# Optimization experiments

Measured on AMD Instinct MI355X. Metric: run time of the kernel, lower is better.

Reference implementation:

```python
import jax, jax.numpy as jnp
import numpy as np

B, N1, N2, E = 8, 32, 32, 256
H = 8                 # num_heads == args.vir_heads
KD = E // H           # key dim per head = 32
HD = E // H           # head dim (value_dim == embed_dim)
L = N1 * N2           # 1024 tokens
SCALING = KD ** -0.5
LN_EPS = 1e-5


def _rel_pos_2d():
    # RetNetRelPosDeform2D with zero offsets (vir_use_deformable=False)
    half = 1.0 / 10000.0 ** jnp.linspace(0.0, 1.0, KD // 2)
    angle = jnp.repeat(half, 2)                                   # (KD,) interleaved pairs
    decay = jnp.log(1.0 - 2.0 ** (-2.0 - 5.0 * jnp.arange(H, dtype=jnp.float32) / H))  # (H,)
    i1 = jnp.arange(N1, dtype=jnp.float32)
    i2 = jnp.arange(N2, dtype=jnp.float32)
    index_k = (i1[:, None] + i2[None, :]).reshape(L)              # (L,)
    sin_k = jnp.sin(index_k[:, None] * angle[None, :])            # (L, KD)
    cos_k = jnp.cos(index_k[:, None] * angle[None, :])
    # zero offsets => index_q == index_k, broadcast over (B, H)
    sin_q = sin_k[None, None]                                     # (1,1,L,KD)
    cos_q = cos_k[None, None]
    # Manhattan distance decay mask on the 2D grid
    d = (jnp.abs(i1[:, None, None, None] - i1[None, None, :, None])
         + jnp.abs(i2[None, :, None, None] - i2[None, None, None, :])).reshape(L, L)
    mask = jnp.exp(d[None, :, :] * decay[:, None, None])          # (H, L, L)
    mask = jnp.nan_to_num(mask)
    mask = mask / jnp.sqrt(mask.sum(-1, keepdims=True))
    return sin_q, cos_q, sin_k, cos_k, mask


def rotate_every_two(x):
    x1 = x[..., ::2]
    x2 = x[..., 1::2]
    return jnp.stack((-x2, x1), axis=-1).reshape(x.shape)


def theta_shift(x, sin, cos):
    return x * cos + rotate_every_two(x) * sin


def setup_inputs() -> dict:
    key = jax.random.key(0)
    ks = jax.random.split(key, 5)
    gain_qkv = 2.0 ** -2.5 * (6.0 / (E + E)) ** 0.5  # xavier_uniform bound scale
    gain_o = 2.0 ** -1 * (6.0 / (E + E)) ** 0.5
    x = jax.random.normal(ks[0], (B, N1, N2, E), dtype=jnp.float32)
    Wq = jax.random.uniform(ks[1], (E, E), jnp.float32, -gain_qkv, gain_qkv)
    Wk = jax.random.uniform(ks[2], (E, E), jnp.float32, -gain_qkv, gain_qkv)
    Wv = jax.random.uniform(ks[3], (E, E), jnp.float32, -gain_qkv, gain_qkv)
    Wo = jax.random.uniform(ks[4], (E, E), jnp.float32, -gain_o, gain_o)
    ln_g = jnp.ones((HD,), jnp.float32)
    ln_b = jnp.zeros((HD,), jnp.float32)
    return {"x": x, "Wq": Wq, "Wk": Wk, "Wv": Wv, "Wo": Wo, "ln_g": ln_g, "ln_b": ln_b}


def reference(x, Wq, Wk, Wv, Wo, ln_g, ln_b):
    sin_q, cos_q, sin_k, cos_k, mask = _rel_pos_2d()
    xf = x.reshape(B, L, E)
    q = (xf @ Wq.T).reshape(B, L, H, KD).transpose(0, 2, 1, 3)    # (B,H,L,KD)
    k = (xf @ Wk.T * SCALING).reshape(B, L, H, KD).transpose(0, 2, 1, 3)
    vr = (xf @ Wv.T).reshape(B, L, H, HD).transpose(0, 2, 1, 3)   # (B,H,L,HD)
    qr = theta_shift(q, sin_q, cos_q)
    kr = theta_shift(k, sin_k[None, None], cos_k[None, None])
    qk = jnp.einsum('bhqd,bhkd->bhqk', qr, kr) * mask[None]       # (B,H,L,L)
    den = jnp.clip(jax.lax.stop_gradient(jnp.abs(qk)).sum(-1, keepdims=True), 1.0, 5e4)
    qk = qk / den
    out = jnp.einsum('bhqk,bhkd->bhqd', qk, vr).transpose(0, 2, 1, 3)  # (B,L,H,HD)
    mu = out.mean(-1, keepdims=True)
    var = out.var(-1, keepdims=True)
    out = (out - mu) / jnp.sqrt(var + LN_EPS) * ln_g + ln_b       # per-head LayerNorm
    out = jax.nn.gelu(out.reshape(B, L, H * HD), approximate=False)
    out = out @ Wo.T
    return out.reshape(B, N1, N2, E)
```

## Files before the change

kernel.cpp:

```cpp
#include <hip/hip_runtime.h>
#include <math.h>

typedef unsigned short u16;
typedef unsigned int u32;
typedef unsigned long long u64;
typedef __bf16 bf16x8 __attribute__((ext_vector_type(8)));
typedef short s16x4 __attribute__((ext_vector_type(4)));
typedef float f32x4 __attribute__((ext_vector_type(4)));

#define SCALING 0.17677669529663687f
#define LOG2E 1.44269504088896f
#define LOG2_10000 13.287712379549449f

__device__ __forceinline__ u16 f2bf(float f) {
    u32 u; __builtin_memcpy(&u, &f, 4);
    u = u + 0x7FFFu + ((u >> 16) & 1u);
    return (u16)(u >> 16);
}
__device__ __forceinline__ u32 fbits(float f) {
    u32 u; __builtin_memcpy(&u, &f, 4); return u;
}
__device__ __forceinline__ u32 pack_bf16(float lo, float hi) {
#if __has_builtin(__builtin_amdgcn_cvt_pk_bf16_f32)
    typedef __bf16 bf16x2_t __attribute__((ext_vector_type(2)));
    bf16x2_t r = __builtin_amdgcn_cvt_pk_bf16_f32(lo, hi);
    u32 u; __builtin_memcpy(&u, &r, 4); return u;
#else
    return __builtin_amdgcn_perm(fbits(hi) + 0x8000u, fbits(lo) + 0x8000u, 0x07060302u);
#endif
}
__device__ __forceinline__ f32x4 mfma16(bf16x8 a, bf16x8 b, f32x4 c) {
    return __builtin_amdgcn_mfma_f32_16x16x32_bf16(a, b, c, 0, 0, 0);
}
__device__ __forceinline__ f32x4 mfma_k16(u64 a, u64 b, f32x4 c) {
#if __has_builtin(__builtin_amdgcn_mfma_f32_16x16x16bf16_1k)
    s16x4 av, bv;
    __builtin_memcpy(&av, &a, 8); __builtin_memcpy(&bv, &b, 8);
    return __builtin_amdgcn_mfma_f32_16x16x16bf16_1k(av, bv, c, 0, 0, 0);
#elif __has_builtin(__builtin_amdgcn_mfma_f32_16x16x16_bf16)
    typedef __bf16 bf16x4_t __attribute__((ext_vector_type(4)));
    bf16x4_t av, bv;
    __builtin_memcpy(&av, &a, 8); __builtin_memcpy(&bv, &b, 8);
    return __builtin_amdgcn_mfma_f32_16x16x16_bf16(av, bv, c, 0, 0, 0);
#else
    f32x4 d = c;
    asm volatile("v_mfma_f32_16x16x16_bf16 %0, %1, %2, %0\n\ts_nop 4"
                 : "+v"(d) : "v"(a), "v"(b));
    return d;
#endif
}
__device__ __forceinline__ float decay_l2(int h) {
    return logf(1.0f - exp2f(-2.0f - 0.625f * (float)h)) * LOG2E;
}

__global__ __launch_bounds__(256) void prep_kernel(
    const float* __restrict__ x,
    const float* __restrict__ Wq, const float* __restrict__ Wk,
    const float* __restrict__ Wv, const float* __restrict__ Wo,
    u16* __restrict__ xb, u16* __restrict__ wb, float2* __restrict__ tc) {
    int bid = blockIdx.x;
    if (bid >= 1152) {
        int idx = (bid - 1152) * 256 + threadIdx.x;
        int l = idx >> 5, d = idx & 31;
        float ang = exp2f(-LOG2_10000 * (1.0f / 15.0f) * (float)(d >> 1));
        float idl = (float)((l >> 5) + (l & 31));
        float sv, cv;
        __sincosf(idl * ang, &sv, &cv);
        tc[idx] = make_float2(cv, (d & 1) ? sv : -sv);
        return;
    }
    const float* src; u16* dst; int off;
    if (bid < 1024) { src = x; dst = xb; off = bid * 2048; }
    else {
        int wsel = (bid - 1024) >> 5;
        src = (wsel == 0) ? Wq : (wsel == 1) ? Wk : (wsel == 2) ? Wv : Wo;
        dst = wb + wsel * 65536;
        off = ((bid - 1024) & 31) * 2048;
    }
    int i = off + threadIdx.x * 8;
    float4 a = *(const float4*)&src[i];
    float4 b = *(const float4*)&src[i + 4];
    int4 t;
    t.x = (int)pack_bf16(a.x, a.y); t.y = (int)pack_bf16(a.z, a.w);
    t.z = (int)pack_bf16(b.x, b.y); t.w = (int)pack_bf16(b.z, b.w);
    *(int4*)&dst[i] = t;
}

template<int MT>
__global__ __launch_bounds__(256) void gemm_bt_kernel(
    const u16* __restrict__ A, const u16* __restrict__ Wb,
    const float2* __restrict__ tc,
    u16* __restrict__ O0, u16* __restrict__ O1, u16* __restrict__ O2,
    float* __restrict__ Of, int mode_base) {
    __shared__ __align__(16) u16 As[64 * MT * 136];
    __shared__ __align__(16) u16 Ws[64 * 136];
    int z = blockIdx.z;
    const u16* W = Wb + z * 65536;
    u16* O = (z == 0) ? O0 : (z == 1) ? O1 : O2;
    int mode = mode_base + z;
    int n0 = blockIdx.x * 64, r0 = blockIdx.y * (64 * MT);
    int tid = threadIdx.x;
    int w = tid >> 6, lane = tid & 63, ln = lane & 15, quad = lane >> 4;
    f32x4 acc[MT][4] = {};
#pragma unroll
    for (int ch = 0; ch < 2; ch++) {
        int k0 = ch * 128;
        if (ch) __syncthreads();
#pragma unroll
        for (int i = 0; i < 4 * MT; i++) {
            int c = tid + i * 256;
            int row = c >> 4, seg = c & 15;
            *(int4*)&As[row * 136 + seg * 8] = *(const int4*)&A[(long)(r0 + row) * 256 + k0 + seg * 8];
        }
#pragma unroll
        for (int i = 0; i < 4; i++) {
            int c = tid + i * 256;
            int row = c >> 4, seg = c & 15;
            *(int4*)&Ws[row * 136 + seg * 8] = *(const int4*)&W[(long)(n0 + row) * 256 + k0 + seg * 8];
        }
        __syncthreads();
#pragma unroll
        for (int kt = 0; kt < 4; kt++) {
            bf16x8 a[MT];
#pragma unroll
            for (int m = 0; m < MT; m++)
                a[m] = *(const bf16x8*)&As[(w * MT * 16 + m * 16 + ln) * 136 + kt * 32 + quad * 8];
#pragma unroll
            for (int nt = 0; nt < 4; nt++) {
                bf16x8 b = *(const bf16x8*)&Ws[(nt * 16 + ln) * 136 + kt * 32 + quad * 8];
#pragma unroll
                for (int m = 0; m < MT; m++)
                    acc[m][nt] = mfma16(a[m], b, acc[m][nt]);
            }
        }
    }
#pragma unroll
    for (int m = 0; m < MT; m++) {
        int rowg = r0 + w * MT * 16 + m * 16 + quad * 4;
        if (mode == 3) {
#pragma unroll
            for (int nt = 0; nt < 4; nt++) {
                int e = n0 + nt * 16 + ln;
#pragma unroll
                for (int r = 0; r < 4; r++)
                    Of[(long)(rowg + r) * 256 + e] = acc[m][nt][r];
            }
            continue;
        }
        float scl = (mode == 1) ? SCALING : 1.0f;
#pragma unroll
        for (int nt = 0; nt < 4; nt++) {
            int e = n0 + nt * 16 + ln;
            int d = e & 31, hh = e >> 5;
#pragma unroll
            for (int r = 0; r < 4; r++) {
                int gi = rowg + r;
                int b = gi >> 10, l = gi & 1023;
                float v = acc[m][nt][r] * scl;
                float p = __shfl_xor(v, 1);
                float res;
                if (mode == 2) {
                    res = v;
                } else {
                    float2 sc = tc[l * 32 + d];
                    res = v * sc.x + p * sc.y;
                }
                O[(((long)(b * 8 + hh)) * 1024 + l) * 32 + d] = f2bf(res);
            }
        }
    }
}

__global__ __launch_bounds__(512) void attn_kernel(
    const u16* __restrict__ qr, const u16* __restrict__ kr, const u16* __restrict__ vr,
    const float* __restrict__ lng, const float* __restrict__ lnb,
    u16* __restrict__ out) {
    __shared__ __align__(16) u16 Qs[256 * 40];
    __shared__ __align__(16) u16 Ks[2][64 * 40];
    __shared__ __align__(16) u32 VtW[2][32 * 36];
    __shared__ float Tt[64];
    __shared__ float Ss[32];
    int p = blockIdx.x + 4 * (blockIdx.y + 8 * blockIdx.z);
    int xcd = p & 7, slot = p >> 3;
    int c = xcd * 8 + (slot >> 2);
    int b = c >> 3, h = c & 7, q0 = (slot & 3) * 256;
    int tid = threadIdx.x, w = tid >> 6, lane = tid & 63, ln = lane & 15, quad = lane >> 4;
    long bh = b * 8 + h;
    const u16* qb = qr + bh * 32768;
    const u16* kb = kr + bh * 32768;
    const u16* vb = vr + bh * 32768;
    float dec = decay_l2(h);
#pragma unroll
    for (int i = 0; i < 2; i++) {
        int cc = tid + i * 512;
        int row = cc >> 2, seg = cc & 3;
        *(int4*)&Qs[row * 40 + seg * 8] = *(const int4*)&qb[(q0 + row) * 32 + seg * 8];
    }
    if (tid < 63) Tt[tid] = exp2f(dec * (float)tid);
    bool isK = (tid < 256);
    int krow = (tid & 255) >> 2, kseg = tid & 3;
    int vt = tid & 255, vp = vt >> 3, vseg = vt & 7;
    int4 kreg; int2 v0, v1;
    if (isK) {
        kreg = *(const int4*)&kb[(long)krow * 32 + kseg * 8];
    } else {
        v0 = *(const int2*)&vb[(long)(vp * 2) * 32 + vseg * 4];
        v1 = *(const int2*)&vb[(long)(vp * 2 + 1) * 32 + vseg * 4];
    }
    __syncthreads();
    bf16x8 aq0 = *(const bf16x8*)&Qs[(w * 32 + ln) * 40 + quad * 8];
    bf16x8 aq1 = *(const bf16x8*)&Qs[(w * 32 + 16 + ln) * 40 + quad * 8];
    int qA = q0 + w * 32 + ln;
    int q1i = qA >> 5;
    int q2i0 = qA & 31, q2i1 = (qA + 16) & 31;
    if (tid < 32) {
        float s = 0.0f;
#pragma unroll
        for (int b2 = 0; b2 < 32; b2++) s += Tt[abs(tid - b2)];
        Ss[tid] = s;
    }
    if (isK) {
        *(int4*)&Ks[0][krow * 40 + kseg * 8] = kreg;
    } else {
        VtW[0][(vseg * 4 + 0) * 36 + vp] = __builtin_amdgcn_perm(v1.x, v0.x, 0x05040100u);
        VtW[0][(vseg * 4 + 1) * 36 + vp] = __builtin_amdgcn_perm(v1.x, v0.x, 0x07060302u);
        VtW[0][(vseg * 4 + 2) * 36 + vp] = __builtin_amdgcn_perm(v1.y, v0.y, 0x05040100u);
        VtW[0][(vseg * 4 + 3) * 36 + vp] = __builtin_amdgcn_perm(v1.y, v0.y, 0x07060302u);
    }
    __syncthreads();
    float rqv0 = rsqrtf(Ss[q1i] * Ss[q2i0]);
    float rqv1 = rsqrtf(Ss[q1i] * Ss[q2i1]);
    float bt[2][2][4];
#pragma unroll
    for (int s2 = 0; s2 < 2; s2++)
#pragma unroll
        for (int r = 0; r < 4; r++) {
            int kk = s2 * 16 + quad * 4 + r;
            bt[0][s2][r] = Tt[abs(q2i0 - kk)] * rqv0;
            bt[1][s2][r] = Tt[abs(q2i1 - kk)] * rqv1;
        }
    f32x4 accO[2][2] = {};
    float den[2] = {0.0f, 0.0f};
    for (int kt = 0; kt < 16; kt++) {
        int cur = kt & 1;
        if (kt < 15) {
            long t1 = (long)(kt + 1) * 64;
            if (isK) {
                kreg = *(const int4*)&kb[(t1 + krow) * 32 + kseg * 8];
            } else {
                v0 = *(const int2*)&vb[(t1 + vp * 2) * 32 + vseg * 4];
                v1 = *(const int2*)&vb[(t1 + vp * 2 + 1) * 32 + vseg * 4];
            }
        }
        float a0 = Tt[abs(q1i - 2 * kt)];
        float a1 = Tt[abs(q1i - 2 * kt - 1)];
        const u16* ksb = &Ks[cur][0];
        const u32* vtb = &VtW[cur][0];
#pragma unroll
        for (int nt = 0; nt < 4; nt++) {
            bf16x8 ak = *(const bf16x8*)&ksb[(nt * 16 + ln) * 40 + quad * 8];
            f32x4 s0 = mfma16(ak, aq0, (f32x4){0.f, 0.f, 0.f, 0.f});
            f32x4 s1 = mfma16(ak, aq1, (f32x4){0.f, 0.f, 0.f, 0.f});
            float aa = (nt & 2) ? a1 : a0;
            u64 av0 = *(const u64*)&vtb[ln * 36 + nt * 8 + quad * 2];
            u64 av1 = *(const u64*)&vtb[(16 + ln) * 36 + nt * 8 + quad * 2];
#pragma unroll
            for (int u = 0; u < 2; u++) {
                f32x4 s = u ? s1 : s0;
                float p0 = s[0] * aa * bt[u][nt & 1][0];
                float p1 = s[1] * aa * bt[u][nt & 1][1];
                float p2 = s[2] * aa * bt[u][nt & 1][2];
                float p3 = s[3] * aa * bt[u][nt & 1][3];
                den[u] += fabsf(p0); den[u] += fabsf(p1);
                den[u] += fabsf(p2); den[u] += fabsf(p3);
                u32 blo = pack_bf16(p0, p1), bhi = pack_bf16(p2, p3);
                u64 bb = ((u64)bhi << 32) | blo;
                accO[u][0] = mfma_k16(av0, bb, accO[u][0]);
                accO[u][1] = mfma_k16(av1, bb, accO[u][1]);
            }
        }
        if (kt < 15) {
            int nb = 1 - cur;
            if (isK) {
                *(int4*)&Ks[nb][krow * 40 + kseg * 8] = kreg;
            } else {
                VtW[nb][(vseg * 4 + 0) * 36 + vp] = __builtin_amdgcn_perm(v1.x, v0.x, 0x05040100u);
                VtW[nb][(vseg * 4 + 1) * 36 + vp] = __builtin_amdgcn_perm(v1.x, v0.x, 0x07060302u);
                VtW[nb][(vseg * 4 + 2) * 36 + vp] = __builtin_amdgcn_perm(v1.y, v0.y, 0x05040100u);
                VtW[nb][(vseg * 4 + 3) * 36 + vp] = __builtin_amdgcn_perm(v1.y, v0.y, 0x07060302u);
            }
            __syncthreads();
        }
    }
#pragma unroll
    for (int u = 0; u < 2; u++) {
        float dn = den[u];
        dn += __shfl_xor(dn, 16);
        dn += __shfl_xor(dn, 32);
        float id = 1.0f / fminf(fmaxf(dn, 1.0f), 50000.0f);
        float o[8];
#pragma unroll
        for (int r = 0; r < 4; r++) { o[r] = accO[u][0][r] * id; o[4 + r] = accO[u][1][r] * id; }
        float s1 = 0.0f, s2 = 0.0f;
#pragma unroll
        for (int i = 0; i < 8; i++) { s1 += o[i]; s2 += o[i] * o[i]; }
        s1 += __shfl_xor(s1, 16); s1 += __shfl_xor(s1, 32);
        s2 += __shfl_xor(s2, 16); s2 += __shfl_xor(s2, 32);
        float mean = s1 * (1.0f / 32.0f);
        float var = s2 * (1.0f / 32.0f) - mean * mean;
        float rstd = rsqrtf(var + 1e-5f);
        float xg[8];
#pragma unroll
        for (int nv = 0; nv < 2; nv++)
#pragma unroll
            for (int r = 0; r < 4; r++) {
                int d = nv * 16 + quad * 4 + r;
                float xv = (o[nv * 4 + r] - mean) * rstd * lng[d] + lnb[d];
                xg[nv * 4 + r] = 0.5f * xv * (1.0f + erff(xv * 0.70710678118654752f));
            }
        int q = qA + u * 16;
        u16* orow = out + ((long)(b * 1024 + q)) * 256 + h * 32;
        int2 st0, st1;
        st0.x = (int)pack_bf16(xg[0], xg[1]); st0.y = (int)pack_bf16(xg[2], xg[3]);
        st1.x = (int)pack_bf16(xg[4], xg[5]); st1.y = (int)pack_bf16(xg[6], xg[7]);
        *(int2*)&orow[quad * 4] = st0;
        *(int2*)&orow[16 + quad * 4] = st1;
    }
}

extern "C" void kernel_launch(void* const* d_in, const int* in_sizes, int n_in,
                              void* d_out, int out_size, void* d_ws, size_t ws_size,
                              hipStream_t stream) {
    const float* x   = (const float*)d_in[0];
    const float* Wq  = (const float*)d_in[1];
    const float* Wk  = (const float*)d_in[2];
    const float* Wv  = (const float*)d_in[3];
    const float* Wo  = (const float*)d_in[4];
    const float* lng = (const float*)d_in[5];
    const float* lnb = (const float*)d_in[6];
    float* outp = (float*)d_out;

    u16* xb    = (u16*)d_ws;
    u16* wb    = xb + 2097152;
    u16* qr    = wb + 262144;
    u16* kr    = qr + 2097152;
    u16* vr    = kr + 2097152;
    u16* attnb = vr + 2097152;
    float2* tc = (float2*)(attnb + 2097152);

    prep_kernel<<<1280, 256, 0, stream>>>(x, Wq, Wk, Wv, Wo, xb, wb, tc);
    gemm_bt_kernel<2><<<dim3(4, 64, 3), 256, 0, stream>>>(xb, wb, tc, qr, kr, vr, nullptr, 0);
    attn_kernel<<<dim3(4, 8, 8), 512, 0, stream>>>(qr, kr, vr, lng, lnb, attnb);
    gemm_bt_kernel<1><<<dim3(4, 128, 1), 256, 0, stream>>>(attnb, wb + 3 * 65536, tc, nullptr, nullptr, nullptr, outp, 3);
}
```

Baseline: 116.8 us.

## Halve attention block size, merge K/V loaders, widen V LDS reads, retile QKV GEMM

The attention kernel now uses 256-thread blocks covering 128 queries each, launched as a plain 8x8x8 grid, so there are twice as many blocks and the XCD-aware block remapping is gone. Every thread now loads both K and V instead of splitting the loaders by thread index. The transposed V tile in shared memory is re-laid out so each lane fetches both MFMA V operands with one 128-bit read. The QKV projection GEMM switches to the smaller-tile template with twice as many blocks. Together these aim to raise occupancy and cut LDS instruction count, at the cost of reloading K/V tiles for twice as many query blocks and losing the L2-locality block ordering.

```diff
diff --git a/kernel.cpp b/kernel.cpp
--- a/kernel.cpp
+++ b/kernel.cpp
@@ -7,6 +7,7 @@
 typedef __bf16 bf16x8 __attribute__((ext_vector_type(8)));
 typedef short s16x4 __attribute__((ext_vector_type(4)));
 typedef float f32x4 __attribute__((ext_vector_type(4)));
+typedef u32 u32x4 __attribute__((ext_vector_type(4)));
 
 #define SCALING 0.17677669529663687f
 #define LOG2E 1.44269504088896f
@@ -171,19 +172,16 @@
     }
 }
 
-__global__ __launch_bounds__(512) void attn_kernel(
+__global__ __launch_bounds__(256) void attn_kernel(
     const u16* __restrict__ qr, const u16* __restrict__ kr, const u16* __restrict__ vr,
     const float* __restrict__ lng, const float* __restrict__ lnb,
     u16* __restrict__ out) {
-    __shared__ __align__(16) u16 Qs[256 * 40];
+    __shared__ __align__(16) u16 Qs[128 * 40];
     __shared__ __align__(16) u16 Ks[2][64 * 40];
-    __shared__ __align__(16) u32 VtW[2][32 * 36];
+    __shared__ __align__(16) u32 VtW[2][16 * 68];
     __shared__ float Tt[64];
     __shared__ float Ss[32];
-    int p = blockIdx.x + 4 * (blockIdx.y + 8 * blockIdx.z);
-    int xcd = p & 7, slot = p >> 3;
-    int c = xcd * 8 + (slot >> 2);
-    int b = c >> 3, h = c & 7, q0 = (slot & 3) * 256;
+    int b = blockIdx.z, h = blockIdx.y, q0 = blockIdx.x * 128;
     int tid = threadIdx.x, w = tid >> 6, lane = tid & 63, ln = lane & 15, quad = lane >> 4;
     long bh = b * 8 + h;
     const u16* qb = qr + bh * 32768;
@@ -192,21 +190,19 @@
     float dec = decay_l2(h);
 #pragma unroll
     for (int i = 0; i < 2; i++) {
-        int cc = tid + i * 512;
+        int cc = tid + i * 256;
         int row = cc >> 2, seg = cc & 3;
         *(int4*)&Qs[row * 40 + seg * 8] = *(const int4*)&qb[(q0 + row) * 32 + seg * 8];
     }
     if (tid < 63) Tt[tid] = exp2f(dec * (float)tid);
-    bool isK = (tid < 256);
-    int krow = (tid & 255) >> 2, kseg = tid & 3;
-    int vt = tid & 255, vp = vt >> 3, vseg = vt & 7;
+    int krow = tid >> 2, kseg = tid & 3;
+    int vp = tid >> 3, vseg = tid & 7;
+    int vrow = (vseg & 3) * 4;
+    int vcol = (vp >> 1) * 4 + (vp & 1) + (vseg >> 2) * 2;
     int4 kreg; int2 v0, v1;
-    if (isK) {
-        kreg = *(const int4*)&kb[(long)krow * 32 + kseg * 8];
-    } else {
-        v0 = *(const int2*)&vb[(long)(vp * 2) * 32 + vseg * 4];
-        v1 = *(const int2*)&vb[(long)(vp * 2 + 1) * 32 + vseg * 4];
-    }
+    kreg = *(const int4*)&kb[(long)krow * 32 + kseg * 8];
+    v0 = *(const int2*)&vb[(long)(vp * 2) * 32 + vseg * 4];
+    v1 = *(const int2*)&vb[(long)(vp * 2 + 1) * 32 + vseg * 4];
     __syncthreads();
     bf16x8 aq0 = *(const bf16x8*)&Qs[(w * 32 + ln) * 40 + quad * 8];
     bf16x8 aq1 = *(const bf16x8*)&Qs[(w * 32 + 16 + ln) * 40 + quad * 8];
@@ -219,13 +215,13 @@
         for (int b2 = 0; b2 < 32; b2++) s += Tt[abs(tid - b2)];
         Ss[tid] = s;
     }
-    if (isK) {
-        *(int4*)&Ks[0][krow * 40 + kseg * 8] = kreg;
-    } else {
-        VtW[0][(vseg * 4 + 0) * 36 + vp] = __builtin_amdgcn_perm(v1.x, v0.x, 0x05040100u);
-        VtW[0][(vseg * 4 + 1) * 36 + vp] = __builtin_amdgcn_perm(v1.x, v0.x, 0x07060302u);
-        VtW[0][(vseg * 4 + 2) * 36 + vp] = __builtin_amdgcn_perm(v1.y, v0.y, 0x05040100u);
-        VtW[0][(vseg * 4 + 3) * 36 + vp] = __builtin_amdgcn_perm(v1.y, v0.y, 0x07060302u);
+    *(int4*)&Ks[0][krow * 40 + kseg * 8] = kreg;
+    {
+        u32* vwb = &VtW[0][0];
+        vwb[(vrow + 0) * 68 + vcol] = __builtin_amdgcn_perm(v1.x, v0.x, 0x05040100u);
+        vwb[(vrow + 1) * 68 + vcol] = __builtin_amdgcn_perm(v1.x, v0.x, 0x07060302u);
+        vwb[(vrow + 2) * 68 + vcol] = __builtin_amdgcn_perm(v1.y, v0.y, 0x05040100u);
+        vwb[(vrow + 3) * 68 + vcol] = __builtin_amdgcn_perm(v1.y, v0.y, 0x07060302u);
     }
     __syncthreads();
     float rqv0 = rsqrtf(Ss[q1i] * Ss[q2i0]);
@@ -245,12 +241,9 @@
         int cur = kt & 1;
         if (kt < 15) {
             long t1 = (long)(kt + 1) * 64;
-            if (isK) {
-                kreg = *(const int4*)&kb[(t1 + krow) * 32 + kseg * 8];
-            } else {
-                v0 = *(const int2*)&vb[(t1 + vp * 2) * 32 + vseg * 4];
-                v1 = *(const int2*)&vb[(t1 + vp * 2 + 1) * 32 + vseg * 4];
-            }
+            kreg = *(const int4*)&kb[(t1 + krow) * 32 + kseg * 8];
+            v0 = *(const int2*)&vb[(t1 + vp * 2) * 32 + vseg * 4];
+            v1 = *(const int2*)&vb[(t1 + vp * 2 + 1) * 32 + vseg * 4];
         }
         float a0 = Tt[abs(q1i - 2 * kt)];
         float a1 = Tt[abs(q1i - 2 * kt - 1)];
@@ -262,8 +255,9 @@
             f32x4 s0 = mfma16(ak, aq0, (f32x4){0.f, 0.f, 0.f, 0.f});
             f32x4 s1 = mfma16(ak, aq1, (f32x4){0.f, 0.f, 0.f, 0.f});
             float aa = (nt & 2) ? a1 : a0;
-            u64 av0 = *(const u64*)&vtb[ln * 36 + nt * 8 + quad * 2];
-            u64 av1 = *(const u64*)&vtb[(16 + ln) * 36 + nt * 8 + quad * 2];
+            u32x4 vv = *(const u32x4*)&vtb[ln * 68 + (nt * 4 + quad) * 4];
+            u64 av0 = ((u64)vv.y << 32) | vv.x;
+            u64 av1 = ((u64)vv.w << 32) | vv.z;
 #pragma unroll
             for (int u = 0; u < 2; u++) {
                 f32x4 s = u ? s1 : s0;
@@ -281,14 +275,12 @@
         }
         if (kt < 15) {
             int nb = 1 - cur;
-            if (isK) {
-                *(int4*)&Ks[nb][krow * 40 + kseg * 8] = kreg;
-            } else {
-                VtW[nb][(vseg * 4 + 0) * 36 + vp] = __builtin_amdgcn_perm(v1.x, v0.x, 0x05040100u);
-                VtW[nb][(vseg * 4 + 1) * 36 + vp] = __builtin_amdgcn_perm(v1.x, v0.x, 0x07060302u);
-                VtW[nb][(vseg * 4 + 2) * 36 + vp] = __builtin_amdgcn_perm(v1.y, v0.y, 0x05040100u);
-                VtW[nb][(vseg * 4 + 3) * 36 + vp] = __builtin_amdgcn_perm(v1.y, v0.y, 0x07060302u);
-            }
+            *(int4*)&Ks[nb][krow * 40 + kseg * 8] = kreg;
+            u32* vwb = &VtW[nb][0];
+            vwb[(vrow + 0) * 68 + vcol] = __builtin_amdgcn_perm(v1.x, v0.x, 0x05040100u);
+            vwb[(vrow + 1) * 68 + vcol] = __builtin_amdgcn_perm(v1.x, v0.x, 0x07060302u);
+            vwb[(vrow + 2) * 68 + vcol] = __builtin_amdgcn_perm(v1.y, v0.y, 0x05040100u);
+            vwb[(vrow + 3) * 68 + vcol] = __builtin_amdgcn_perm(v1.y, v0.y, 0x07060302u);
             __syncthreads();
         }
     }
@@ -349,7 +341,7 @@
     float2* tc = (float2*)(attnb + 2097152);
 
     prep_kernel<<<1280, 256, 0, stream>>>(x, Wq, Wk, Wv, Wo, xb, wb, tc);
-    gemm_bt_kernel<2><<<dim3(4, 64, 3), 256, 0, stream>>>(xb, wb, tc, qr, kr, vr, nullptr, 0);
-    attn_kernel<<<dim3(4, 8, 8), 512, 0, stream>>>(qr, kr, vr, lng, lnb, attnb);
+    gemm_bt_kernel<1><<<dim3(4, 128, 3), 256, 0, stream>>>(xb, wb, tc, qr, kr, vr, nullptr, 0);
+    attn_kernel<<<dim3(8, 8, 8), 256, 0, stream>>>(qr, kr, vr, lng, lnb, attnb);
     gemm_bt_kernel<1><<<dim3(4, 128, 1), 256, 0, stream>>>(attnb, wb + 3 * 65536, tc, nullptr, nullptr, nullptr, outp, 3);
 }
```

Result: no change. 115.6 us (-1.1%).
